# Optimization experiments

Hardware: AMD Instinct MI355X
Metric: run time of the kernel (lower is better)

## Reference

```python
import jax, jax.numpy as jnp
import numpy as np

B, T = 2, 2048
D_MODEL = 1024
N_LAYERS = 2
VOCAB = 256
BLOCK = 2048
LOCAL = 128
STRIDE = 256
NHEAD = D_MODEL // 64  # 16
HEAD_DIM = D_MODEL // NHEAD  # 64
LN_EPS = 1e-5


def setup_inputs() -> dict:
    key = jax.random.key(0)
    ks = jax.random.split(key, 16)
    L, d = N_LAYERS, D_MODEL

    def g(k, shape, scale=0.02):
        return (jax.random.normal(k, shape, dtype=jnp.float32) * scale)

    return {
        "x": jax.random.randint(ks[0], (B, T), 0, VOCAB),
        "embed": g(ks[1], (VOCAB, d)),
        "pos_embed": g(ks[2], (BLOCK, d)),
        # per-layer weights stacked on leading L axis; Linear as y = x @ W + b
        "Wq": g(ks[3], (L, d, d)), "bq": jnp.zeros((L, d), jnp.float32),
        "Wk": g(ks[4], (L, d, d)), "bk": jnp.zeros((L, d), jnp.float32),
        "Wv": g(ks[5], (L, d, d)), "bv": jnp.zeros((L, d), jnp.float32),
        "Wo": g(ks[6], (L, d, d)), "bo": jnp.zeros((L, d), jnp.float32),
        "g1": jnp.ones((L, d), jnp.float32), "be1": jnp.zeros((L, d), jnp.float32),
        "W1": g(ks[7], (L, d, 4 * d)), "bf1": jnp.zeros((L, 4 * d), jnp.float32),
        "W2": g(ks[8], (L, 4 * d, d)), "bf2": jnp.zeros((L, d), jnp.float32),
        "g2": jnp.ones((L, d), jnp.float32), "be2": jnp.zeros((L, d), jnp.float32),
        "gf": jnp.ones((d,), jnp.float32), "bef": jnp.zeros((d,), jnp.float32),
        "Whead": g(ks[9], (d, VOCAB)),
    }


def _ln(x, gamma, beta):
    mu = jnp.mean(x, axis=-1, keepdims=True)
    var = jnp.mean(jnp.square(x - mu), axis=-1, keepdims=True)
    return (x - mu) * jax.lax.rsqrt(var + LN_EPS) * gamma + beta


def _sparse_mask(t):
    # allowed[i, j] = True if token i may attend to token j
    i = jnp.arange(t)[:, None]
    j = jnp.arange(t)[None, :]
    causal = j <= i
    local = (i - j) <= LOCAL
    glob = (j % STRIDE) == 0
    return causal & (local | glob)


def _sparse_attn(q, k, v, allowed):
    # q, k, v: [B, T, D] -> [B, H, T, hd]
    b, t, d = q.shape
    def split(x):
        return x.reshape(b, t, NHEAD, HEAD_DIM).transpose(0, 2, 1, 3)
    q, k, v = split(q), split(k), split(v)
    scale = HEAD_DIM ** -0.5
    scores = jnp.einsum("bhqd,bhkd->bhqk", q, k) * scale
    scores = jnp.where(allowed[None, None], scores, -jnp.inf)
    attn = jax.nn.softmax(scores, axis=-1)  # every row has j=i allowed -> no NaN
    out = jnp.einsum("bhqk,bhkd->bhqd", attn, v)
    return out.transpose(0, 2, 1, 3).reshape(b, t, d)


def reference(x, embed, pos_embed, Wq, bq, Wk, bk, Wv, bv, Wo, bo,
              g1, be1, W1, bf1, W2, bf2, g2, be2, gf, bef, Whead):
    b, t = x.shape
    h = embed[x] + pos_embed[jnp.arange(t)][None]
    allowed = _sparse_mask(t)
    for l in range(N_LAYERS):
        h_n = _ln(h, g1[l], be1[l])
        q = h_n @ Wq[l] + bq[l]
        k = h_n @ Wk[l] + bk[l]
        v = h_n @ Wv[l] + bv[l]
        attn_out = _sparse_attn(q, k, v, allowed)
        h = h + (attn_out @ Wo[l] + bo[l])
        h2 = _ln(h, g2[l], be2[l])
        ffn = jax.nn.gelu(h2 @ W1[l] + bf1[l], approximate=False) @ W2[l] + bf2[l]
        h = h + ffn
    h = _ln(h, gf, bef)
    return h @ Whead
```

## Files before the change

kernel.cpp:

```cpp
#include <hip/hip_runtime.h>
#include <hip/hip_bf16.h>

#define BB 2
#define TT 2048
#define DD 1024
#define FF 4096
#define VV 256
#define HH 16
#define HD 64
#define MM (BB * TT)
#define LOCAL_W 128
#define STRIDE_G 256
#define QS 3072

typedef short s16x8 __attribute__((ext_vector_type(8)));
typedef __bf16 bf16x8 __attribute__((ext_vector_type(8)));
typedef float f32x4 __attribute__((ext_vector_type(4)));

#define WAITVM(N) asm volatile("s_waitcnt vmcnt(" #N ")" ::: "memory")
#define CFENCE asm volatile("" ::: "memory")

__device__ __forceinline__ float b2f(unsigned short u) {
  return __builtin_bit_cast(float, (unsigned int)u << 16);
}
__device__ __forceinline__ unsigned short f2b(float f) {
  __hip_bfloat16 h = __float2bfloat16(f);
  return __builtin_bit_cast(unsigned short, h);
}
__device__ __forceinline__ void gl_lds16(const unsigned short* g, unsigned short* l) {
  __builtin_amdgcn_global_load_lds(
      (const __attribute__((address_space(1))) void*)g,
      (__attribute__((address_space(3))) void*)l, 16, 0, 0);
}
__device__ __forceinline__ bf16x8 ldsr(const unsigned short* p) {
  return __builtin_bit_cast(bf16x8, *(const s16x8*)p);
}

__global__ __launch_bounds__(256) void transpose_k(const float* __restrict__ W,
                                                   unsigned short* __restrict__ WT,
                                                   int K, int N) {
  __shared__ float t[32][33];
  const int n0 = blockIdx.x * 32, k0 = blockIdx.y * 32;
  const int tx = threadIdx.x, ty = threadIdx.y;
  for (int r = ty; r < 32; r += 8) t[r][tx] = W[(size_t)(k0 + r) * N + n0 + tx];
  __syncthreads();
  for (int r = ty; r < 32; r += 8)
    WT[(size_t)(n0 + r) * K + k0 + tx] = f2b(t[tx][r]);
}

__global__ __launch_bounds__(256) void concat_bias(const float* __restrict__ bq,
                                                   const float* __restrict__ bk,
                                                   const float* __restrict__ bv,
                                                   float* __restrict__ bcat) {
  const int i = blockIdx.x * 256 + threadIdx.x;
  const int l = i / QS, j = i - l * QS;
  float v;
  if (j < DD) v = bq[l * DD + j];
  else if (j < 2 * DD) v = bk[l * DD + j - DD];
  else v = bv[l * DD + j - 2 * DD];
  bcat[i] = v;
}

__global__ __launch_bounds__(256) void embed_kernel(const int* __restrict__ x,
                                                    const float* __restrict__ emb,
                                                    const float* __restrict__ pos,
                                                    float* __restrict__ h) {
  const int row = blockIdx.x;
  const int c = threadIdx.x * 4;
  const int tok = x[row];
  const int t = row & (TT - 1);
  float4 e = *(const float4*)&emb[(size_t)tok * DD + c];
  float4 p = *(const float4*)&pos[(size_t)t * DD + c];
  e.x += p.x; e.y += p.y; e.z += p.z; e.w += p.w;
  *(float4*)&h[(size_t)row * DD + c] = e;
}

__global__ __launch_bounds__(256) void ln_kernel(const float* __restrict__ x,
                                                 const float* __restrict__ g,
                                                 const float* __restrict__ be,
                                                 unsigned short* __restrict__ out) {
  const int row = blockIdx.x;
  const int tid = threadIdx.x;
  const float4 v = *(const float4*)&x[(size_t)row * DD + tid * 4];
  float s = v.x + v.y + v.z + v.w;
  float sq = v.x * v.x + v.y * v.y + v.z * v.z + v.w * v.w;
#pragma unroll
  for (int off = 32; off; off >>= 1) {
    s += __shfl_xor(s, off);
    sq += __shfl_xor(sq, off);
  }
  __shared__ float ss[4], ssq[4];
  const int w = tid >> 6, lane = tid & 63;
  if (lane == 0) { ss[w] = s; ssq[w] = sq; }
  __syncthreads();
  s = ss[0] + ss[1] + ss[2] + ss[3];
  sq = ssq[0] + ssq[1] + ssq[2] + ssq[3];
  const float mean = s * (1.0f / DD);
  const float var = sq * (1.0f / DD) - mean * mean;
  const float rstd = rsqrtf(var + 1e-5f);
  const float4 gv = *(const float4*)&g[tid * 4];
  const float4 bv = *(const float4*)&be[tid * 4];
  ushort4 o;
  o.x = f2b((v.x - mean) * rstd * gv.x + bv.x);
  o.y = f2b((v.y - mean) * rstd * gv.y + bv.y);
  o.z = f2b((v.z - mean) * rstd * gv.z + bv.z);
  o.w = f2b((v.w - mean) * rstd * gv.w + bv.w);
  *(ushort4*)&out[(size_t)row * DD + tid * 4] = o;
}

__global__ __launch_bounds__(256) void ln_red(float* __restrict__ hio,
                                              const float* __restrict__ parts,
                                              const float* __restrict__ bias,
                                              const float* __restrict__ g,
                                              const float* __restrict__ be,
                                              unsigned short* __restrict__ out) {
  const int row = blockIdx.x;
  const int tid = threadIdx.x;
  const size_t base = (size_t)row * DD + tid * 4;
  f32x4 v = *(const f32x4*)&hio[base];
  v += *(const f32x4*)&bias[tid * 4];
  v += *(const f32x4*)&parts[base];
  v += *(const f32x4*)&parts[(size_t)MM * DD + base];
  *(f32x4*)&hio[base] = v;
  float s = v[0] + v[1] + v[2] + v[3];
  float sq = v[0] * v[0] + v[1] * v[1] + v[2] * v[2] + v[3] * v[3];
#pragma unroll
  for (int off = 32; off; off >>= 1) {
    s += __shfl_xor(s, off);
    sq += __shfl_xor(sq, off);
  }
  __shared__ float ss[4], ssq[4];
  const int w = tid >> 6, lane = tid & 63;
  if (lane == 0) { ss[w] = s; ssq[w] = sq; }
  __syncthreads();
  s = ss[0] + ss[1] + ss[2] + ss[3];
  sq = ssq[0] + ssq[1] + ssq[2] + ssq[3];
  const float mean = s * (1.0f / DD);
  const float var = sq * (1.0f / DD) - mean * mean;
  const float rstd = rsqrtf(var + 1e-5f);
  const float4 gv = *(const float4*)&g[tid * 4];
  const float4 bv = *(const float4*)&be[tid * 4];
  ushort4 o;
  o.x = f2b((v[0] - mean) * rstd * gv.x + bv.x);
  o.y = f2b((v[1] - mean) * rstd * gv.y + bv.y);
  o.z = f2b((v[2] - mean) * rstd * gv.z + bv.z);
  o.w = f2b((v[3] - mean) * rstd * gv.w + bv.w);
  *(ushort4*)&out[(size_t)row * DD + tid * 4] = o;
}

template <int EPI>
__global__ __launch_bounds__(512, 2) void gemm8p(const unsigned short* __restrict__ A,
                                                 const unsigned short* __restrict__ BT,
                                                 const float* __restrict__ bias,
                                                 unsigned short* __restrict__ outp,
                                                 int M, int N, int K, int nbx) {
  __shared__ __align__(16) unsigned short lds[65536];
  const int tid = threadIdx.x;
  const int lane = tid & 63;
  const int w = tid >> 6;
  const int nwg = gridDim.x;
  const int orig = blockIdx.x;
  const int wg = (orig & 7) * (nwg >> 3) + (orig >> 3);
  const int n0 = (wg % nbx) * 256, m0 = (wg / nbx) * 256;
  const int wm = w >> 2, wn = w & 3;
  f32x4 acc[8][4] = {};

  const unsigned short* aSrc[2];
  const unsigned short* bSrc[2];
  int dstO[2];
#pragma unroll
  for (int i = 0; i < 2; i++) {
    const int s = tid + (i << 9);
    const int row = s >> 2, sc = s & 3;
    const int l = sc ^ ((row >> 1) & 3);
    aSrc[i] = &A[(size_t)(m0 + row) * K + l * 8];
    bSrc[i] = &BT[(size_t)(n0 + row) * K + l * 8];
    dstO[i] = s * 8;
  }
  auto STAGE = [&](int tb, int ks, int obase) {
    const int kt = (tb << 6) + (ks << 5);
    const int so = obase + ks * 16384;
#pragma unroll
    for (int i = 0; i < 2; i++) {
      gl_lds16(aSrc[i] + kt, &lds[so + dstO[i]]);
      gl_lds16(bSrc[i] + kt, &lds[so + 8192 + dstO[i]]);
    }
  };

  const int rA = lane & 15, cr = lane >> 4;
  const int rowA0 = wm * 128 + rA;
  const int rowB0 = wn * 64 + rA;
  const int aAddr0 = rowA0 * 32 + ((cr ^ ((rowA0 >> 1) & 3)) << 3);
  const int bAddr0 = 8192 + rowB0 * 32 + ((cr ^ ((rowB0 >> 1) & 3)) << 3);

  const int NT = K >> 6;
  STAGE(0, 0, 0);
  STAGE(0, 1, 0);

  auto TILE = [&](int bufc, int tb, bool notlast) {
    const int bb = bufc << 15;
    const int ob = (bufc ^ 1) << 15;
    bf16x8 bfr[4], af[4];
    WAITVM(4);
    __builtin_amdgcn_s_barrier();
    CFENCE;
    if (notlast) STAGE(tb + 1, 0, ob);
#pragma unroll
    for (int n = 0; n < 4; n++) bfr[n] = ldsr(&lds[bb + bAddr0 + n * 512]);
#pragma unroll
    for (int i = 0; i < 4; i++) af[i] = ldsr(&lds[bb + aAddr0 + i * 512]);
    __builtin_amdgcn_s_setprio(1);
#pragma unroll
    for (int i = 0; i < 4; i++)
#pragma unroll
      for (int n = 0; n < 4; n++)
        acc[i][n] = __builtin_amdgcn_mfma_f32_16x16x32_bf16(af[i], bfr[n], acc[i][n], 0, 0, 0);
    __builtin_amdgcn_s_setprio(0);
#pragma unroll
    for (int i = 0; i < 4; i++) af[i] = ldsr(&lds[bb + aAddr0 + (4 + i) * 512]);
    __builtin_amdgcn_s_setprio(1);
#pragma unroll
    for (int i = 0; i < 4; i++)
#pragma unroll
      for (int n = 0; n < 4; n++)
        acc[4 + i][n] = __builtin_amdgcn_mfma_f32_16x16x32_bf16(af[i], bfr[n], acc[4 + i][n], 0, 0, 0);
    __builtin_amdgcn_s_setprio(0);
    if (notlast) { WAITVM(4); } else { WAITVM(0); }
    __builtin_amdgcn_s_barrier();
    CFENCE;
    if (notlast) STAGE(tb + 1, 1, ob);
#pragma unroll
    for (int n = 0; n < 4; n++) bfr[n] = ldsr(&lds[bb + 16384 + bAddr0 + n * 512]);
#pragma unroll
    for (int i = 0; i < 4; i++) af[i] = ldsr(&lds[bb + 16384 + aAddr0 + i * 512]);
    __builtin_amdgcn_s_setprio(1);
#pragma unroll
    for (int i = 0; i < 4; i++)
#pragma unroll
      for (int n = 0; n < 4; n++)
        acc[i][n] = __builtin_amdgcn_mfma_f32_16x16x32_bf16(af[i], bfr[n], acc[i][n], 0, 0, 0);
    __builtin_amdgcn_s_setprio(0);
#pragma unroll
    for (int i = 0; i < 4; i++) af[i] = ldsr(&lds[bb + 16384 + aAddr0 + (4 + i) * 512]);
    __builtin_amdgcn_s_setprio(1);
#pragma unroll
    for (int i = 0; i < 4; i++)
#pragma unroll
      for (int n = 0; n < 4; n++)
        acc[4 + i][n] = __builtin_amdgcn_mfma_f32_16x16x32_bf16(af[i], bfr[n], acc[4 + i][n], 0, 0, 0);
    __builtin_amdgcn_s_setprio(0);
  };

  for (int it = 0; it < NT; it += 2) {
    TILE(0, it, true);
    TILE(1, it + 1, it + 2 < NT);
  }

  const int r0 = (lane >> 4) * 4;
  const int cc = lane & 15;
#pragma unroll
  for (int m = 0; m < 8; m++) {
#pragma unroll
    for (int n = 0; n < 4; n++) {
#pragma unroll
      for (int r = 0; r < 4; r++) {
        const int row = m0 + wm * 128 + m * 16 + r0 + r;
        const int col = n0 + wn * 64 + n * 16 + cc;
        float val = acc[m][n][r] + bias[col];
        if (EPI == 3) {
          float u = val * (0.7978845608f + 0.0356774081f * val * val);
          u = fminf(u, 10.0f);
          const float e = __expf(2.0f * u);
          val = val * e / (e + 1.0f);
        }
        outp[(size_t)row * N + col] = f2b(val);
      }
    }
  }
}

__global__ __launch_bounds__(512, 2) void gemm_dw(const unsigned short* __restrict__ A,
                                                  const unsigned short* __restrict__ BT,
                                                  float* __restrict__ partial,
                                                  int M, int N, int K, int nbx, int nwg2,
                                                  int ksub) {
  __shared__ __align__(16) unsigned short lds[49152];
  const int tid = threadIdx.x;
  const int lane = tid & 63;
  const int w = tid >> 6;
  const int nwg = gridDim.x;
  const int orig = blockIdx.x;
  const int wg = (orig & 7) * (nwg >> 3) + (orig >> 3);
  const int ks = wg / nwg2;
  const int rem = wg - ks * nwg2;
  const int n0 = (rem % nbx) * 128;
  const int m0 = (rem / nbx) * 256;
  const int kb = ks * ksub;
  const int wm = w >> 2, wn = w & 3;
  f32x4 acc[8][2] = {};

  const unsigned short* aSrc[2];
  const unsigned short* bSrc;
  int dstA[2], dstB;
#pragma unroll
  for (int i = 0; i < 2; i++) {
    const int s = tid + (i << 9);
    const int row = s >> 2, sc = s & 3;
    const int l = sc ^ ((row >> 1) & 3);
    aSrc[i] = &A[(size_t)(m0 + row) * K + kb + l * 8];
    dstA[i] = s * 8;
  }
  {
    const int row = tid >> 2, sc = tid & 3;
    const int l = sc ^ ((row >> 1) & 3);
    bSrc = &BT[(size_t)(n0 + row) * K + kb + l * 8];
    dstB = 8192 + tid * 8;
  }
  auto STAGE = [&](int tb, int kss, int obase) {
    const int kt = (tb << 6) + (kss << 5);
    const int so = obase + kss * 12288;
    gl_lds16(aSrc[0] + kt, &lds[so + dstA[0]]);
    gl_lds16(aSrc[1] + kt, &lds[so + dstA[1]]);
    gl_lds16(bSrc + kt, &lds[so + dstB]);
  };

  const int rA = lane & 15, cr = lane >> 4;
  const int rowA0 = wm * 128 + rA;
  const int rowB0 = wn * 32 + rA;
  const int aAddr0 = rowA0 * 32 + ((cr ^ ((rowA0 >> 1) & 3)) << 3);
  const int bAddr0 = 8192 + rowB0 * 32 + ((cr ^ ((rowB0 >> 1) & 3)) << 3);

  const int NT = ksub >> 6;
  STAGE(0, 0, 0);
  STAGE(0, 1, 0);

  auto TILE = [&](int bufc, int tb, bool notlast) {
    const int bb = bufc * 24576;
    const int ob = (bufc ^ 1) * 24576;
    bf16x8 bfr[2], af[4];
    WAITVM(3);
    __builtin_amdgcn_s_barrier();
    CFENCE;
    if (notlast) STAGE(tb + 1, 0, ob);
#pragma unroll
    for (int n = 0; n < 2; n++) bfr[n] = ldsr(&lds[bb + bAddr0 + n * 512]);
#pragma unroll
    for (int i = 0; i < 4; i++) af[i] = ldsr(&lds[bb + aAddr0 + i * 512]);
    __builtin_amdgcn_s_setprio(1);
#pragma unroll
    for (int i = 0; i < 4; i++)
#pragma unroll
      for (int n = 0; n < 2; n++)
        acc[i][n] = __builtin_amdgcn_mfma_f32_16x16x32_bf16(af[i], bfr[n], acc[i][n], 0, 0, 0);
    __builtin_amdgcn_s_setprio(0);
#pragma unroll
    for (int i = 0; i < 4; i++) af[i] = ldsr(&lds[bb + aAddr0 + (4 + i) * 512]);
    __builtin_amdgcn_s_setprio(1);
#pragma unroll
    for (int i = 0; i < 4; i++)
#pragma unroll
      for (int n = 0; n < 2; n++)
        acc[4 + i][n] = __builtin_amdgcn_mfma_f32_16x16x32_bf16(af[i], bfr[n], acc[4 + i][n], 0, 0, 0);
    __builtin_amdgcn_s_setprio(0);
    if (notlast) { WAITVM(3); } else { WAITVM(0); }
    __builtin_amdgcn_s_barrier();
    CFENCE;
    if (notlast) STAGE(tb + 1, 1, ob);
#pragma unroll
    for (int n = 0; n < 2; n++) bfr[n] = ldsr(&lds[bb + 12288 + bAddr0 + n * 512]);
#pragma unroll
    for (int i = 0; i < 4; i++) af[i] = ldsr(&lds[bb + 12288 + aAddr0 + i * 512]);
    __builtin_amdgcn_s_setprio(1);
#pragma unroll
    for (int i = 0; i < 4; i++)
#pragma unroll
      for (int n = 0; n < 2; n++)
        acc[i][n] = __builtin_amdgcn_mfma_f32_16x16x32_bf16(af[i], bfr[n], acc[i][n], 0, 0, 0);
    __builtin_amdgcn_s_setprio(0);
#pragma unroll
    for (int i = 0; i < 4; i++) af[i] = ldsr(&lds[bb + 12288 + aAddr0 + (4 + i) * 512]);
    __builtin_amdgcn_s_setprio(1);
#pragma unroll
    for (int i = 0; i < 4; i++)
#pragma unroll
      for (int n = 0; n < 2; n++)
        acc[4 + i][n] = __builtin_amdgcn_mfma_f32_16x16x32_bf16(af[i], bfr[n], acc[4 + i][n], 0, 0, 0);
    __builtin_amdgcn_s_setprio(0);
  };

  for (int it = 0; it < NT; it += 2) {
    TILE(0, it, true);
    TILE(1, it + 1, it + 2 < NT);
  }

  float* pout = partial + (size_t)ks * M * N;
  const int r0 = (lane >> 4) * 4;
  const int cc = lane & 15;
#pragma unroll
  for (int m = 0; m < 8; m++)
#pragma unroll
    for (int n = 0; n < 2; n++)
#pragma unroll
      for (int r = 0; r < 4; r++) {
        const int row = m0 + wm * 128 + m * 16 + r0 + r;
        const int col = n0 + wn * 32 + n * 16 + cc;
        pout[(size_t)row * N + col] = acc[m][n][r];
      }
}

__global__ __launch_bounds__(512, 2) void gemm_p(const unsigned short* __restrict__ A,
                                                 const unsigned short* __restrict__ BT,
                                                 float* __restrict__ outp,
                                                 int M, int N, int K, int nbx, int nwg2,
                                                 int ksub) {
  constexpr int BM = 128;
  __shared__ __align__(16) unsigned short lds[4][BM * 64];
  const int tid = threadIdx.x;
  const int lane = tid & 63;
  const int w = tid >> 6;
  const int nwg = gridDim.x;
  const int orig = blockIdx.x;
  const int wg = (orig & 7) * (nwg >> 3) + (orig >> 3);
  const int ks = wg / nwg2;
  const int rem = wg - ks * nwg2;
  const int n0 = (rem % nbx) * BM;
  const int m0 = (rem / nbx) * BM;
  const int kb = ks * ksub;
  const int wm = w >> 2, wn = w & 3;
  f32x4 acc[4][2] = {};

  auto STAGE = [&](int t) {
    const int b = t & 3;
    const int kt = kb + (t << 5);
    const int s = tid;
    const int row = s >> 2, sc = s & 3;
    const int c = sc ^ ((row >> 1) & 3);
    gl_lds16(&A[(size_t)(m0 + row) * K + kt + c * 8], &lds[b][s * 8]);
    gl_lds16(&BT[(size_t)(n0 + row) * K + kt + c * 8], &lds[b][BM * 32 + s * 8]);
  };

  const int NT = ksub >> 5;
  STAGE(0); STAGE(1); STAGE(2);

  for (int t = 0; t < NT; ++t) {
    const int ahead = NT - 1 - t;
    if (ahead >= 2) WAITVM(4); else if (ahead == 1) WAITVM(2); else WAITVM(0);
    __builtin_amdgcn_s_barrier();
    CFENCE;
    if (t + 3 < NT) STAGE(t + 3);
    const int b = t & 3;
    const int rA = lane & 15, cr = lane >> 4;
    bf16x8 af[4], bfr[2];
#pragma unroll
    for (int m = 0; m < 4; m++) {
      const int row = wm * 64 + m * 16 + rA;
      af[m] = ldsr(&lds[b][row * 32 + ((cr ^ ((row >> 1) & 3)) << 3)]);
    }
#pragma unroll
    for (int n = 0; n < 2; n++) {
      const int row = wn * 32 + n * 16 + rA;
      bfr[n] = ldsr(&lds[b][BM * 32 + row * 32 + ((cr ^ ((row >> 1) & 3)) << 3)]);
    }
    __builtin_amdgcn_s_setprio(1);
#pragma unroll
    for (int m = 0; m < 4; m++)
#pragma unroll
      for (int n = 0; n < 2; n++)
        acc[m][n] = __builtin_amdgcn_mfma_f32_16x16x32_bf16(af[m], bfr[n], acc[m][n], 0, 0, 0);
    __builtin_amdgcn_s_setprio(0);
  }

  const int r0 = (lane >> 4) * 4;
  const int cc = lane & 15;
  float* pout = outp + (size_t)ks * M * N;
#pragma unroll
  for (int m = 0; m < 4; m++)
#pragma unroll
    for (int n = 0; n < 2; n++)
#pragma unroll
      for (int r = 0; r < 4; r++) {
        const int row = m0 + wm * 64 + m * 16 + r0 + r;
        const int col = n0 + wn * 32 + n * 16 + cc;
        pout[(size_t)row * N + col] = acc[m][n][r];
      }
}

template <int NP>
__global__ __launch_bounds__(256) void reduce_k(float* __restrict__ dst,
                                                const float* __restrict__ parts,
                                                size_t total) {
  const size_t i = ((size_t)blockIdx.x * 256 + threadIdx.x) * 4;
  if (i >= total) return;
  f32x4 acc = {};
#pragma unroll
  for (int p = 0; p < NP; p++) acc += *(const f32x4*)&parts[(size_t)p * total + i];
  *(f32x4*)&dst[i] = acc;
}

#define QT 16
#define KT 32
#define NTMAX 6
#define KP 72
#define PP 40

__global__ __launch_bounds__(256) void attn_mfma(const unsigned short* __restrict__ qkv,
                                                 unsigned short* __restrict__ outg) {
  __shared__ __align__(16) unsigned short kvs[4][KT * KP];
  __shared__ __align__(16) unsigned short pls[4][QT * PP];
  const int tid = threadIdx.x;
  const int wid = tid >> 6, lane = tid & 63;
  const int qgrp = blockIdx.x & 31;
  const int bh = blockIdx.x >> 5;
  const int h = bh & (HH - 1), b = bh >> 4;
  const size_t baseq = (size_t)b * TT * QS + (size_t)h * HD;
  const size_t baseo = (size_t)b * TT * DD + (size_t)h * HD;
  const int i0 = qgrp * 64 + wid * 16;
  const int g = lane >> 4;
  const int c = lane & 15;

  const int i0b = qgrp * 64 + 48;
  const int ka0b = (i0b > 128) ? ((i0b - 128) & ~31) : 0;
  const int nlb = ((i0b + 16 - ka0b) + 31) >> 5;
  const int neb = (ka0b + 255) >> 8;
  const int ka0 = (i0 > 128) ? ((i0 - 128) & ~31) : 0;
  const int ne = (ka0 + 255) >> 8;

  const s16x8 qf0 = *(const s16x8*)&qkv[baseq + (size_t)(i0 + c) * QS + g * 8];
  const s16x8 qf1 = *(const s16x8*)&qkv[baseq + (size_t)(i0 + c) * QS + 32 + g * 8];

  f32x4 sc[NTMAX][2];
  float smax[4] = {-1e30f, -1e30f, -1e30f, -1e30f};

#pragma unroll
  for (int t = 0; t < NTMAX; t++) {
    if (t > nlb) continue;
    const bool isg = (t == 0);
    if (isg && neb == 0) continue;
    const int kt0 = ka0 + (t - 1) * 32;
#pragma unroll
    for (int it = 0; it < 4; it++) {
      const int row = it * 8 + (lane >> 3);
      const int ch = lane & 7;
      const int j = isg ? ((row < ne) ? row * STRIDE_G : 0) : (kt0 + row);
      *(s16x8*)&kvs[wid][row * KP + ch * 8] =
          *(const s16x8*)&qkv[baseq + DD + (size_t)j * QS + ch * 8];
    }
    __syncthreads();
#pragma unroll
    for (int half = 0; half < 2; half++) {
      const int key = half * 16 + c;
      const bf16x8 kb0 = __builtin_bit_cast(bf16x8, *(const s16x8*)&kvs[wid][key * KP + g * 8]);
      const bf16x8 kb1 = __builtin_bit_cast(bf16x8, *(const s16x8*)&kvs[wid][key * KP + 32 + g * 8]);
      f32x4 a = {};
      a = __builtin_amdgcn_mfma_f32_16x16x32_bf16(__builtin_bit_cast(bf16x8, qf0), kb0, a, 0, 0, 0);
      a = __builtin_amdgcn_mfma_f32_16x16x32_bf16(__builtin_bit_cast(bf16x8, qf1), kb1, a, 0, 0, 0);
#pragma unroll
      for (int r = 0; r < 4; r++) {
        const int i = i0 + g * 4 + r;
        bool ok;
        if (isg) {
          ok = (key < ne);
        } else {
          const int j = kt0 + key;
          ok = (j <= i) && (((i - j) <= LOCAL_W) || ((j & (STRIDE_G - 1)) == 0));
        }
        const float s = ok ? a[r] * 0.125f : -1e30f;
        sc[t][half][r] = s;
        smax[r] = fmaxf(smax[r], s);
      }
    }
    __syncthreads();
  }
#pragma unroll
  for (int r = 0; r < 4; r++)
#pragma unroll
    for (int off = 8; off; off >>= 1)
      smax[r] = fmaxf(smax[r], __shfl_xor(smax[r], off));

  f32x4 o[4] = {};
  float lsum[4] = {0.f, 0.f, 0.f, 0.f};
#pragma unroll
  for (int t = 0; t < NTMAX; t++) {
    if (t > nlb) continue;
    const bool isg = (t == 0);
    if (isg && neb == 0) continue;
    const int kt0 = ka0 + (t - 1) * 32;
#pragma unroll
    for (int it = 0; it < 4; it++) {
      const int row = it * 8 + (lane >> 3);
      const int ch = lane & 7;
      const int j = isg ? ((row < ne) ? row * STRIDE_G : 0) : (kt0 + row);
      *(s16x8*)&kvs[wid][row * KP + ch * 8] =
          *(const s16x8*)&qkv[baseq + 2 * DD + (size_t)j * QS + ch * 8];
    }
#pragma unroll
    for (int half = 0; half < 2; half++)
#pragma unroll
      for (int r = 0; r < 4; r++) {
        const float p = __expf(sc[t][half][r] - smax[r]);
        lsum[r] += p;
        pls[wid][(g * 4 + r) * PP + half * 16 + c] = f2b(p);
      }
    __syncthreads();
    const bf16x8 pa = __builtin_bit_cast(bf16x8, *(const s16x8*)&pls[wid][c * PP + g * 8]);
#pragma unroll
    for (int d0 = 0; d0 < 4; d0++) {
      s16x8 bv;
#pragma unroll
      for (int e = 0; e < 8; e++)
        bv[e] = (short)kvs[wid][(g * 8 + e) * KP + d0 * 16 + c];
      o[d0] = __builtin_amdgcn_mfma_f32_16x16x32_bf16(pa, __builtin_bit_cast(bf16x8, bv), o[d0], 0, 0, 0);
    }
    __syncthreads();
  }
#pragma unroll
  for (int r = 0; r < 4; r++)
#pragma unroll
    for (int off = 8; off; off >>= 1)
      lsum[r] += __shfl_xor(lsum[r], off);
#pragma unroll
  for (int d0 = 0; d0 < 4; d0++)
#pragma unroll
    for (int r = 0; r < 4; r++)
      outg[baseo + (size_t)(i0 + g * 4 + r) * DD + d0 * 16 + c] = f2b(o[d0][r] / lsum[r]);
}

extern "C" void kernel_launch(void* const* d_in, const int* in_sizes, int n_in,
                              void* d_out, int out_size, void* d_ws, size_t ws_size,
                              hipStream_t stream) {
  const int* x = (const int*)d_in[0];
  const float* embed = (const float*)d_in[1];
  const float* pos = (const float*)d_in[2];
  const float* Wq = (const float*)d_in[3];
  const float* bq = (const float*)d_in[4];
  const float* Wk = (const float*)d_in[5];
  const float* bk = (const float*)d_in[6];
  const float* Wv = (const float*)d_in[7];
  const float* bv = (const float*)d_in[8];
  const float* Wo = (const float*)d_in[9];
  const float* bo = (const float*)d_in[10];
  const float* g1 = (const float*)d_in[11];
  const float* be1 = (const float*)d_in[12];
  const float* W1 = (const float*)d_in[13];
  const float* bf1 = (const float*)d_in[14];
  const float* W2 = (const float*)d_in[15];
  const float* bf2 = (const float*)d_in[16];
  const float* g2 = (const float*)d_in[17];
  const float* be2 = (const float*)d_in[18];
  const float* gf = (const float*)d_in[19];
  const float* bef = (const float*)d_in[20];
  const float* Whead = (const float*)d_in[21];

  char* ws = (char*)d_ws;
  size_t off = 0;
  auto alloc = [&](size_t bytes) -> void* {
    void* p = ws + off;
    off += (bytes + 255) & ~(size_t)255;
    return p;
  };
  unsigned short* WqkvT = (unsigned short*)alloc((size_t)2 * QS * DD * 2);
  unsigned short* WoT = (unsigned short*)alloc((size_t)2 * DD * DD * 2);
  unsigned short* W1T = (unsigned short*)alloc((size_t)2 * DD * FF * 2);
  unsigned short* W2T = (unsigned short*)alloc((size_t)2 * DD * FF * 2);
  unsigned short* WheadT = (unsigned short*)alloc((size_t)DD * VV * 2);
  float* bcat = (float*)alloc((size_t)2 * QS * 4);
  float* h = (float*)alloc((size_t)MM * DD * 4);
  unsigned short* hn = (unsigned short*)alloc((size_t)MM * DD * 2);
  unsigned short* qkvb = (unsigned short*)alloc((size_t)MM * QS * 2);
  unsigned short* attnb = (unsigned short*)alloc((size_t)MM * DD * 2);
  unsigned short* mid = (unsigned short*)alloc((size_t)MM * FF * 2);
  float* ffn2p = (float*)qkvb;
  float* oprojp = (float*)mid;
  float* headp = (float*)mid;
  (void)ws_size;

  const dim3 tb(32, 8);
  for (int l = 0; l < 2; l++) {
    const size_t wo = (size_t)l * DD * DD;
    const size_t wf = (size_t)l * DD * FF;
    transpose_k<<<dim3(DD / 32, DD / 32), tb, 0, stream>>>(Wq + wo, WqkvT + (size_t)l * QS * DD, DD, DD);
    transpose_k<<<dim3(DD / 32, DD / 32), tb, 0, stream>>>(Wk + wo, WqkvT + ((size_t)l * QS + DD) * DD, DD, DD);
    transpose_k<<<dim3(DD / 32, DD / 32), tb, 0, stream>>>(Wv + wo, WqkvT + ((size_t)l * QS + 2 * DD) * DD, DD, DD);
    transpose_k<<<dim3(DD / 32, DD / 32), tb, 0, stream>>>(Wo + wo, WoT + wo, DD, DD);
    transpose_k<<<dim3(FF / 32, DD / 32), tb, 0, stream>>>(W1 + wf, W1T + wf, DD, FF);
    transpose_k<<<dim3(DD / 32, FF / 32), tb, 0, stream>>>(W2 + wf, W2T + wf, FF, DD);
  }
  transpose_k<<<dim3(VV / 32, DD / 32), tb, 0, stream>>>(Whead, WheadT, DD, VV);
  concat_bias<<<24, 256, 0, stream>>>(bq, bk, bv, bcat);

  embed_kernel<<<MM, 256, 0, stream>>>(x, embed, pos, h);
  ln_kernel<<<MM, 256, 0, stream>>>(h, g1, be1, hn);

  for (int l = 0; l < 2; l++) {
    const size_t wo = (size_t)l * DD * DD;
    const size_t wf = (size_t)l * DD * FF;
    gemm8p<1><<<(QS / 256) * (MM / 256), 512, 0, stream>>>(
        hn, WqkvT + (size_t)l * QS * DD, bcat + l * QS, qkvb, MM, QS, DD, QS / 256);
    attn_mfma<<<BB * HH * (TT / 64), 256, 0, stream>>>(qkvb, attnb);
    gemm_dw<<<2 * (DD / 128) * (MM / 256), 512, 0, stream>>>(
        attnb, WoT + wo, oprojp, MM, DD, DD, DD / 128, (DD / 128) * (MM / 256), DD / 2);
    ln_red<<<MM, 256, 0, stream>>>(h, oprojp, bo + l * DD, g2 + l * DD, be2 + l * DD, hn);
    gemm8p<3><<<(FF / 256) * (MM / 256), 512, 0, stream>>>(
        hn, W1T + wf, bf1 + l * FF, mid, MM, FF, DD, FF / 256);
    gemm_dw<<<2 * (DD / 128) * (MM / 256), 512, 0, stream>>>(
        mid, W2T + wf, ffn2p, MM, DD, FF, DD / 128, (DD / 128) * (MM / 256), FF / 2);
    if (l == 0)
      ln_red<<<MM, 256, 0, stream>>>(h, ffn2p, bf2, g1 + DD, be1 + DD, hn);
    else
      ln_red<<<MM, 256, 0, stream>>>(h, ffn2p, bf2 + DD, gf, bef, hn);
  }
  gemm_p<<<4 * (VV / 128) * (MM / 128), 512, 0, stream>>>(
      hn, WheadT, headp, MM, VV, DD, VV / 128, (VV / 128) * (MM / 128), DD / 4);
  reduce_k<4><<<(MM * VV) / 1024, 256, 0, stream>>>(
      (float*)d_out, headp, (size_t)MM * VV);
}
```

Measured before the change: 440.7 us.

## Deepen GEMM prefetch and split A/B staging across half-tile barriers

Restructures the software pipeline in the two bf16 GEMM kernels so global-to-LDS loads run a half-tile further ahead, with three k-substages in flight instead of two. A and B staging are split and issued at separate points between the MFMA groups, guarded by extra workgroup barriers. The aim is to hide more global-load latency and spread load issue between compute bursts. The cost is more s_barrier instructions per tile and tighter vmcnt accounting, which could add sync overhead or hazards if the counts are off.

After: 558.7 us. 1.27x slower.

```diff
diff --git a/kernel.cpp b/kernel.cpp
--- a/kernel.cpp
+++ b/kernel.cpp
@@ -177,14 +177,17 @@
     bSrc[i] = &BT[(size_t)(n0 + row) * K + l * 8];
     dstO[i] = s * 8;
   }
-  auto STAGE = [&](int tb, int ks, int obase) {
-    const int kt = (tb << 6) + (ks << 5);
-    const int so = obase + ks * 16384;
-#pragma unroll
-    for (int i = 0; i < 2; i++) {
-      gl_lds16(aSrc[i] + kt, &lds[so + dstO[i]]);
-      gl_lds16(bSrc[i] + kt, &lds[so + 8192 + dstO[i]]);
-    }
+  auto STAGE_A = [&](int u, int ks) {
+    const int kt = (u << 6) + (ks << 5);
+    const int so = ((u & 1) << 15) + ks * 16384;
+    gl_lds16(aSrc[0] + kt, &lds[so + dstO[0]]);
+    gl_lds16(aSrc[1] + kt, &lds[so + dstO[1]]);
+  };
+  auto STAGE_B = [&](int u, int ks) {
+    const int kt = (u << 6) + (ks << 5);
+    const int so = ((u & 1) << 15) + ks * 16384;
+    gl_lds16(bSrc[0] + kt, &lds[so + 8192 + dstO[0]]);
+    gl_lds16(bSrc[1] + kt, &lds[so + 8192 + dstO[1]]);
   };
 
   const int rA = lane & 15, cr = lane >> 4;
@@ -194,17 +197,17 @@
   const int bAddr0 = 8192 + rowB0 * 32 + ((cr ^ ((rowB0 >> 1) & 3)) << 3);
 
   const int NT = K >> 6;
-  STAGE(0, 0, 0);
-  STAGE(0, 1, 0);
-
-  auto TILE = [&](int bufc, int tb, bool notlast) {
-    const int bb = bufc << 15;
-    const int ob = (bufc ^ 1) << 15;
+  STAGE_A(0, 0); STAGE_B(0, 0);
+  STAGE_A(0, 1); STAGE_B(0, 1);
+  STAGE_A(1, 0); STAGE_B(1, 0);
+
+  auto TILE = [&](int bb, int t) {
+    const bool s1 = (t + 1) < NT;
+    const bool s2 = (t + 2) < NT;
     bf16x8 bfr[4], af[4];
-    WAITVM(4);
-    __builtin_amdgcn_s_barrier();
-    CFENCE;
-    if (notlast) STAGE(tb + 1, 0, ob);
+    if (s1) WAITVM(8); else WAITVM(4);
+    if (s1) STAGE_A(t + 1, 1);
+    __builtin_amdgcn_s_barrier(); CFENCE;
 #pragma unroll
     for (int n = 0; n < 4; n++) bfr[n] = ldsr(&lds[bb + bAddr0 + n * 512]);
 #pragma unroll
@@ -216,8 +219,11 @@
       for (int n = 0; n < 4; n++)
         acc[i][n] = __builtin_amdgcn_mfma_f32_16x16x32_bf16(af[i], bfr[n], acc[i][n], 0, 0, 0);
     __builtin_amdgcn_s_setprio(0);
+    __builtin_amdgcn_s_barrier();
 #pragma unroll
     for (int i = 0; i < 4; i++) af[i] = ldsr(&lds[bb + aAddr0 + (4 + i) * 512]);
+    if (s1) STAGE_B(t + 1, 1);
+    __builtin_amdgcn_s_barrier(); CFENCE;
     __builtin_amdgcn_s_setprio(1);
 #pragma unroll
     for (int i = 0; i < 4; i++)
@@ -225,10 +231,10 @@
       for (int n = 0; n < 4; n++)
         acc[4 + i][n] = __builtin_amdgcn_mfma_f32_16x16x32_bf16(af[i], bfr[n], acc[4 + i][n], 0, 0, 0);
     __builtin_amdgcn_s_setprio(0);
-    if (notlast) { WAITVM(4); } else { WAITVM(0); }
-    __builtin_amdgcn_s_barrier();
-    CFENCE;
-    if (notlast) STAGE(tb + 1, 1, ob);
+    __builtin_amdgcn_s_barrier();
+    if (s1) WAITVM(8); else WAITVM(0);
+    if (s2) STAGE_A(t + 2, 0);
+    __builtin_amdgcn_s_barrier(); CFENCE;
 #pragma unroll
     for (int n = 0; n < 4; n++) bfr[n] = ldsr(&lds[bb + 16384 + bAddr0 + n * 512]);
 #pragma unroll
@@ -240,8 +246,11 @@
       for (int n = 0; n < 4; n++)
         acc[i][n] = __builtin_amdgcn_mfma_f32_16x16x32_bf16(af[i], bfr[n], acc[i][n], 0, 0, 0);
     __builtin_amdgcn_s_setprio(0);
+    __builtin_amdgcn_s_barrier();
 #pragma unroll
     for (int i = 0; i < 4; i++) af[i] = ldsr(&lds[bb + 16384 + aAddr0 + (4 + i) * 512]);
+    if (s2) STAGE_B(t + 2, 0);
+    __builtin_amdgcn_s_barrier(); CFENCE;
     __builtin_amdgcn_s_setprio(1);
 #pragma unroll
     for (int i = 0; i < 4; i++)
@@ -249,11 +258,12 @@
       for (int n = 0; n < 4; n++)
         acc[4 + i][n] = __builtin_amdgcn_mfma_f32_16x16x32_bf16(af[i], bfr[n], acc[4 + i][n], 0, 0, 0);
     __builtin_amdgcn_s_setprio(0);
+    __builtin_amdgcn_s_barrier();
   };
 
   for (int it = 0; it < NT; it += 2) {
-    TILE(0, it, true);
-    TILE(1, it + 1, it + 2 < NT);
+    TILE(0, it);
+    TILE(32768, it + 1);
   }
 
   const int r0 = (lane >> 4) * 4;
@@ -316,11 +326,15 @@
     bSrc = &BT[(size_t)(n0 + row) * K + kb + l * 8];
     dstB = 8192 + tid * 8;
   }
-  auto STAGE = [&](int tb, int kss, int obase) {
-    const int kt = (tb << 6) + (kss << 5);
-    const int so = obase + kss * 12288;
+  auto STAGE_A = [&](int u, int kss) {
+    const int kt = (u << 6) + (kss << 5);
+    const int so = (u & 1) * 24576 + kss * 12288;
     gl_lds16(aSrc[0] + kt, &lds[so + dstA[0]]);
     gl_lds16(aSrc[1] + kt, &lds[so + dstA[1]]);
+  };
+  auto STAGE_B = [&](int u, int kss) {
+    const int kt = (u << 6) + (kss << 5);
+    const int so = (u & 1) * 24576 + kss * 12288;
     gl_lds16(bSrc + kt, &lds[so + dstB]);
   };
 
@@ -331,17 +345,17 @@
   const int bAddr0 = 8192 + rowB0 * 32 + ((cr ^ ((rowB0 >> 1) & 3)) << 3);
 
   const int NT = ksub >> 6;
-  STAGE(0, 0, 0);
-  STAGE(0, 1, 0);
-
-  auto TILE = [&](int bufc, int tb, bool notlast) {
-    const int bb = bufc * 24576;
-    const int ob = (bufc ^ 1) * 24576;
+  STAGE_A(0, 0); STAGE_B(0, 0);
+  STAGE_A(0, 1); STAGE_B(0, 1);
+  STAGE_A(1, 0); STAGE_B(1, 0);
+
+  auto TILE = [&](int bb, int t) {
+    const bool s1 = (t + 1) < NT;
+    const bool s2 = (t + 2) < NT;
     bf16x8 bfr[2], af[4];
-    WAITVM(3);
-    __builtin_amdgcn_s_barrier();
-    CFENCE;
-    if (notlast) STAGE(tb + 1, 0, ob);
+    if (s1) WAITVM(6); else WAITVM(3);
+    if (s1) STAGE_A(t + 1, 1);
+    __builtin_amdgcn_s_barrier(); CFENCE;
 #pragma unroll
     for (int n = 0; n < 2; n++) bfr[n] = ldsr(&lds[bb + bAddr0 + n * 512]);
 #pragma unroll
@@ -353,8 +367,11 @@
       for (int n = 0; n < 2; n++)
         acc[i][n] = __builtin_amdgcn_mfma_f32_16x16x32_bf16(af[i], bfr[n], acc[i][n], 0, 0, 0);
     __builtin_amdgcn_s_setprio(0);
+    __builtin_amdgcn_s_barrier();
 #pragma unroll
     for (int i = 0; i < 4; i++) af[i] = ldsr(&lds[bb + aAddr0 + (4 + i) * 512]);
+    if (s1) STAGE_B(t + 1, 1);
+    __builtin_amdgcn_s_barrier(); CFENCE;
     __builtin_amdgcn_s_setprio(1);
 #pragma unroll
     for (int i = 0; i < 4; i++)
@@ -362,10 +379,10 @@
       for (int n = 0; n < 2; n++)
         acc[4 + i][n] = __builtin_amdgcn_mfma_f32_16x16x32_bf16(af[i], bfr[n], acc[4 + i][n], 0, 0, 0);
     __builtin_amdgcn_s_setprio(0);
-    if (notlast) { WAITVM(3); } else { WAITVM(0); }
-    __builtin_amdgcn_s_barrier();
-    CFENCE;
-    if (notlast) STAGE(tb + 1, 1, ob);
+    __builtin_amdgcn_s_barrier();
+    if (s1) WAITVM(6); else WAITVM(0);
+    if (s2) STAGE_A(t + 2, 0);
+    __builtin_amdgcn_s_barrier(); CFENCE;
 #pragma unroll
     for (int n = 0; n < 2; n++) bfr[n] = ldsr(&lds[bb + 12288 + bAddr0 + n * 512]);
 #pragma unroll
@@ -377,8 +394,11 @@
       for (int n = 0; n < 2; n++)
         acc[i][n] = __builtin_amdgcn_mfma_f32_16x16x32_bf16(af[i], bfr[n], acc[i][n], 0, 0, 0);
     __builtin_amdgcn_s_setprio(0);
+    __builtin_amdgcn_s_barrier();
 #pragma unroll
     for (int i = 0; i < 4; i++) af[i] = ldsr(&lds[bb + 12288 + aAddr0 + (4 + i) * 512]);
+    if (s2) STAGE_B(t + 2, 0);
+    __builtin_amdgcn_s_barrier(); CFENCE;
     __builtin_amdgcn_s_setprio(1);
 #pragma unroll
     for (int i = 0; i < 4; i++)
@@ -386,11 +406,12 @@
       for (int n = 0; n < 2; n++)
         acc[4 + i][n] = __builtin_amdgcn_mfma_f32_16x16x32_bf16(af[i], bfr[n], acc[4 + i][n], 0, 0, 0);
     __builtin_amdgcn_s_setprio(0);
+    __builtin_amdgcn_s_barrier();
   };
 
   for (int it = 0; it < NT; it += 2) {
-    TILE(0, it, true);
-    TILE(1, it + 1, it + 2 < NT);
+    TILE(0, it);
+    TILE(24576, it + 1);
   }
 
   float* pout = partial + (size_t)ks * M * N;
```

## Batch weight transposes, fuse embed with LN, use 256x128 tiles for QKV GEMM

Applied to the files above, without the earlier changes.

Folds the 13 per-layer weight transpose launches into 5 by indexing layer and matrix through blockIdx.z. Merges the embedding add with the first layernorm so h is written once and not read back. Moves the QKV projection from the 256x256 gemm8p kernel to a templated gemm_dw with a bf16+bias epilogue and 128-wide N tiles, giving 384 workgroups instead of 192 for better CU fill, at the cost of more A-tile reloads.

After: 434.7 us. About the same (-1.4%).

```diff
diff --git a/kernel.cpp b/kernel.cpp
--- a/kernel.cpp
+++ b/kernel.cpp
@@ -38,14 +38,35 @@
 
 __global__ __launch_bounds__(256) void transpose_k(const float* __restrict__ W,
                                                    unsigned short* __restrict__ WT,
-                                                   int K, int N) {
+                                                   int K, int N,
+                                                   size_t sstride, size_t dstride) {
   __shared__ float t[32][33];
+  const int z = blockIdx.z;
+  W += (size_t)z * sstride;
+  WT += (size_t)z * dstride;
   const int n0 = blockIdx.x * 32, k0 = blockIdx.y * 32;
   const int tx = threadIdx.x, ty = threadIdx.y;
   for (int r = ty; r < 32; r += 8) t[r][tx] = W[(size_t)(k0 + r) * N + n0 + tx];
   __syncthreads();
   for (int r = ty; r < 32; r += 8)
     WT[(size_t)(n0 + r) * K + k0 + tx] = f2b(t[tx][r]);
+}
+
+__global__ __launch_bounds__(256) void qkv_t(const float* __restrict__ Wq,
+                                             const float* __restrict__ Wk,
+                                             const float* __restrict__ Wv,
+                                             unsigned short* __restrict__ WT) {
+  __shared__ float t[32][33];
+  const int z = blockIdx.z;
+  const int l = z / 3, which = z % 3;
+  const float* W = (which == 0 ? Wq : which == 1 ? Wk : Wv) + (size_t)l * DD * DD;
+  unsigned short* D = WT + ((size_t)l * QS + which * DD) * DD;
+  const int n0 = blockIdx.x * 32, k0 = blockIdx.y * 32;
+  const int tx = threadIdx.x, ty = threadIdx.y;
+  for (int r = ty; r < 32; r += 8) t[r][tx] = W[(size_t)(k0 + r) * DD + n0 + tx];
+  __syncthreads();
+  for (int r = ty; r < 32; r += 8)
+    D[(size_t)(n0 + r) * DD + k0 + tx] = f2b(t[tx][r]);
 }
 
 __global__ __launch_bounds__(256) void concat_bias(const float* __restrict__ bq,
@@ -61,67 +82,20 @@
   bcat[i] = v;
 }
 
-__global__ __launch_bounds__(256) void embed_kernel(const int* __restrict__ x,
-                                                    const float* __restrict__ emb,
-                                                    const float* __restrict__ pos,
-                                                    float* __restrict__ h) {
+__global__ __launch_bounds__(256) void embed_ln(const int* __restrict__ x,
+                                                const float* __restrict__ emb,
+                                                const float* __restrict__ pos,
+                                                const float* __restrict__ g,
+                                                const float* __restrict__ be,
+                                                float* __restrict__ h,
+                                                unsigned short* __restrict__ out) {
   const int row = blockIdx.x;
-  const int c = threadIdx.x * 4;
+  const int tid = threadIdx.x;
   const int tok = x[row];
   const int t = row & (TT - 1);
-  float4 e = *(const float4*)&emb[(size_t)tok * DD + c];
-  float4 p = *(const float4*)&pos[(size_t)t * DD + c];
-  e.x += p.x; e.y += p.y; e.z += p.z; e.w += p.w;
-  *(float4*)&h[(size_t)row * DD + c] = e;
-}
-
-__global__ __launch_bounds__(256) void ln_kernel(const float* __restrict__ x,
-                                                 const float* __restrict__ g,
-                                                 const float* __restrict__ be,
-                                                 unsigned short* __restrict__ out) {
-  const int row = blockIdx.x;
-  const int tid = threadIdx.x;
-  const float4 v = *(const float4*)&x[(size_t)row * DD + tid * 4];
-  float s = v.x + v.y + v.z + v.w;
-  float sq = v.x * v.x + v.y * v.y + v.z * v.z + v.w * v.w;
-#pragma unroll
-  for (int off = 32; off; off >>= 1) {
-    s += __shfl_xor(s, off);
-    sq += __shfl_xor(sq, off);
-  }
-  __shared__ float ss[4], ssq[4];
-  const int w = tid >> 6, lane = tid & 63;
-  if (lane == 0) { ss[w] = s; ssq[w] = sq; }
-  __syncthreads();
-  s = ss[0] + ss[1] + ss[2] + ss[3];
-  sq = ssq[0] + ssq[1] + ssq[2] + ssq[3];
-  const float mean = s * (1.0f / DD);
-  const float var = sq * (1.0f / DD) - mean * mean;
-  const float rstd = rsqrtf(var + 1e-5f);
-  const float4 gv = *(const float4*)&g[tid * 4];
-  const float4 bv = *(const float4*)&be[tid * 4];
-  ushort4 o;
-  o.x = f2b((v.x - mean) * rstd * gv.x + bv.x);
-  o.y = f2b((v.y - mean) * rstd * gv.y + bv.y);
-  o.z = f2b((v.z - mean) * rstd * gv.z + bv.z);
-  o.w = f2b((v.w - mean) * rstd * gv.w + bv.w);
-  *(ushort4*)&out[(size_t)row * DD + tid * 4] = o;
-}
-
-__global__ __launch_bounds__(256) void ln_red(float* __restrict__ hio,
-                                              const float* __restrict__ parts,
-                                              const float* __restrict__ bias,
-                                              const float* __restrict__ g,
-                                              const float* __restrict__ be,
-                                              unsigned short* __restrict__ out) {
-  const int row = blockIdx.x;
-  const int tid = threadIdx.x;
-  const size_t base = (size_t)row * DD + tid * 4;
-  f32x4 v = *(const f32x4*)&hio[base];
-  v += *(const f32x4*)&bias[tid * 4];
-  v += *(const f32x4*)&parts[base];
-  v += *(const f32x4*)&parts[(size_t)MM * DD + base];
-  *(f32x4*)&hio[base] = v;
+  f32x4 v = *(const f32x4*)&emb[(size_t)tok * DD + tid * 4];
+  v += *(const f32x4*)&pos[(size_t)t * DD + tid * 4];
+  *(f32x4*)&h[(size_t)row * DD + tid * 4] = v;
   float s = v[0] + v[1] + v[2] + v[3];
   float sq = v[0] * v[0] + v[1] * v[1] + v[2] * v[2] + v[3] * v[3];
 #pragma unroll
@@ -148,6 +122,46 @@
   *(ushort4*)&out[(size_t)row * DD + tid * 4] = o;
 }
 
+__global__ __launch_bounds__(256) void ln_red(float* __restrict__ hio,
+                                              const float* __restrict__ parts,
+                                              const float* __restrict__ bias,
+                                              const float* __restrict__ g,
+                                              const float* __restrict__ be,
+                                              unsigned short* __restrict__ out) {
+  const int row = blockIdx.x;
+  const int tid = threadIdx.x;
+  const size_t base = (size_t)row * DD + tid * 4;
+  f32x4 v = *(const f32x4*)&hio[base];
+  v += *(const f32x4*)&bias[tid * 4];
+  v += *(const f32x4*)&parts[base];
+  v += *(const f32x4*)&parts[(size_t)MM * DD + base];
+  *(f32x4*)&hio[base] = v;
+  float s = v[0] + v[1] + v[2] + v[3];
+  float sq = v[0] * v[0] + v[1] * v[1] + v[2] * v[2] + v[3] * v[3];
+#pragma unroll
+  for (int off = 32; off; off >>= 1) {
+    s += __shfl_xor(s, off);
+    sq += __shfl_xor(sq, off);
+  }
+  __shared__ float ss[4], ssq[4];
+  const int w = tid >> 6, lane = tid & 63;
+  if (lane == 0) { ss[w] = s; ssq[w] = sq; }
+  __syncthreads();
+  s = ss[0] + ss[1] + ss[2] + ss[3];
+  sq = ssq[0] + ssq[1] + ssq[2] + ssq[3];
+  const float mean = s * (1.0f / DD);
+  const float var = sq * (1.0f / DD) - mean * mean;
+  const float rstd = rsqrtf(var + 1e-5f);
+  const float4 gv = *(const float4*)&g[tid * 4];
+  const float4 bv = *(const float4*)&be[tid * 4];
+  ushort4 o;
+  o.x = f2b((v[0] - mean) * rstd * gv.x + bv.x);
+  o.y = f2b((v[1] - mean) * rstd * gv.y + bv.y);
+  o.z = f2b((v[2] - mean) * rstd * gv.z + bv.z);
+  o.w = f2b((v[3] - mean) * rstd * gv.w + bv.w);
+  *(ushort4*)&out[(size_t)row * DD + tid * 4] = o;
+}
+
 template <int EPI>
 __global__ __launch_bounds__(512, 2) void gemm8p(const unsigned short* __restrict__ A,
                                                  const unsigned short* __restrict__ BT,
@@ -279,9 +293,11 @@
   }
 }
 
+template <int EPI>
 __global__ __launch_bounds__(512, 2) void gemm_dw(const unsigned short* __restrict__ A,
                                                   const unsigned short* __restrict__ BT,
-                                                  float* __restrict__ partial,
+                                                  const float* __restrict__ bias,
+                                                  void* __restrict__ outp,
                                                   int M, int N, int K, int nbx, int nwg2,
                                                   int ksub) {
   __shared__ __align__(16) unsigned short lds[49152];
@@ -393,7 +409,6 @@
     TILE(1, it + 1, it + 2 < NT);
   }
 
-  float* pout = partial + (size_t)ks * M * N;
   const int r0 = (lane >> 4) * 4;
   const int cc = lane & 15;
 #pragma unroll
@@ -404,7 +419,12 @@
       for (int r = 0; r < 4; r++) {
         const int row = m0 + wm * 128 + m * 16 + r0 + r;
         const int col = n0 + wn * 32 + n * 16 + cc;
-        pout[(size_t)row * N + col] = acc[m][n][r];
+        const size_t idx = (size_t)row * N + col;
+        if (EPI == 0) {
+          ((float*)outp)[(size_t)ks * M * N + idx] = acc[m][n][r];
+        } else {
+          ((unsigned short*)outp)[idx] = f2b(acc[m][n][r] + bias[col]);
+        }
       }
 }
 
@@ -675,35 +695,34 @@
   (void)ws_size;
 
   const dim3 tb(32, 8);
+  qkv_t<<<dim3(DD / 32, DD / 32, 6), tb, 0, stream>>>(Wq, Wk, Wv, WqkvT);
+  transpose_k<<<dim3(DD / 32, DD / 32, 2), tb, 0, stream>>>(Wo, WoT, DD, DD,
+                                                            (size_t)DD * DD, (size_t)DD * DD);
+  transpose_k<<<dim3(FF / 32, DD / 32, 2), tb, 0, stream>>>(W1, W1T, DD, FF,
+                                                            (size_t)DD * FF, (size_t)DD * FF);
+  transpose_k<<<dim3(DD / 32, FF / 32, 2), tb, 0, stream>>>(W2, W2T, FF, DD,
+                                                            (size_t)DD * FF, (size_t)DD * FF);
+  transpose_k<<<dim3(VV / 32, DD / 32, 1), tb, 0, stream>>>(Whead, WheadT, DD, VV, 0, 0);
+  concat_bias<<<24, 256, 0, stream>>>(bq, bk, bv, bcat);
+
+  embed_ln<<<MM, 256, 0, stream>>>(x, embed, pos, g1, be1, h, hn);
+
   for (int l = 0; l < 2; l++) {
     const size_t wo = (size_t)l * DD * DD;
     const size_t wf = (size_t)l * DD * FF;
-    transpose_k<<<dim3(DD / 32, DD / 32), tb, 0, stream>>>(Wq + wo, WqkvT + (size_t)l * QS * DD, DD, DD);
-    transpose_k<<<dim3(DD / 32, DD / 32), tb, 0, stream>>>(Wk + wo, WqkvT + ((size_t)l * QS + DD) * DD, DD, DD);
-    transpose_k<<<dim3(DD / 32, DD / 32), tb, 0, stream>>>(Wv + wo, WqkvT + ((size_t)l * QS + 2 * DD) * DD, DD, DD);
-    transpose_k<<<dim3(DD / 32, DD / 32), tb, 0, stream>>>(Wo + wo, WoT + wo, DD, DD);
-    transpose_k<<<dim3(FF / 32, DD / 32), tb, 0, stream>>>(W1 + wf, W1T + wf, DD, FF);
-    transpose_k<<<dim3(DD / 32, FF / 32), tb, 0, stream>>>(W2 + wf, W2T + wf, FF, DD);
-  }
-  transpose_k<<<dim3(VV / 32, DD / 32), tb, 0, stream>>>(Whead, WheadT, DD, VV);
-  concat_bias<<<24, 256, 0, stream>>>(bq, bk, bv, bcat);
-
-  embed_kernel<<<MM, 256, 0, stream>>>(x, embed, pos, h);
-  ln_kernel<<<MM, 256, 0, stream>>>(h, g1, be1, hn);
-
-  for (int l = 0; l < 2; l++) {
-    const size_t wo = (size_t)l * DD * DD;
-    const size_t wf = (size_t)l * DD * FF;
-    gemm8p<1><<<(QS / 256) * (MM / 256), 512, 0, stream>>>(
-        hn, WqkvT + (size_t)l * QS * DD, bcat + l * QS, qkvb, MM, QS, DD, QS / 256);
+    gemm_dw<1><<<(QS / 128) * (MM / 256), 512, 0, stream>>>(
+        hn, WqkvT + (size_t)l * QS * DD, bcat + l * QS, qkvb,
+        MM, QS, DD, QS / 128, (QS / 128) * (MM / 256), DD);
     attn_mfma<<<BB * HH * (TT / 64), 256, 0, stream>>>(qkvb, attnb);
-    gemm_dw<<<2 * (DD / 128) * (MM / 256), 512, 0, stream>>>(
-        attnb, WoT + wo, oprojp, MM, DD, DD, DD / 128, (DD / 128) * (MM / 256), DD / 2);
+    gemm_dw<0><<<2 * (DD / 128) * (MM / 256), 512, 0, stream>>>(
+        attnb, WoT + wo, nullptr, oprojp,
+        MM, DD, DD, DD / 128, (DD / 128) * (MM / 256), DD / 2);
     ln_red<<<MM, 256, 0, stream>>>(h, oprojp, bo + l * DD, g2 + l * DD, be2 + l * DD, hn);
     gemm8p<3><<<(FF / 256) * (MM / 256), 512, 0, stream>>>(
         hn, W1T + wf, bf1 + l * FF, mid, MM, FF, DD, FF / 256);
-    gemm_dw<<<2 * (DD / 128) * (MM / 256), 512, 0, stream>>>(
-        mid, W2T + wf, ffn2p, MM, DD, FF, DD / 128, (DD / 128) * (MM / 256), FF / 2);
+    gemm_dw<0><<<2 * (DD / 128) * (MM / 256), 512, 0, stream>>>(
+        mid, W2T + wf, nullptr, ffn2p,
+        MM, DD, FF, DD / 128, (DD / 128) * (MM / 256), FF / 2);
     if (l == 0)
       ln_red<<<MM, 256, 0, stream>>>(h, ffn2p, bf2, g1 + DD, be1 + DD, hn);
     else
```
